# Kernel tuning notes

Measured on AMD Instinct MI355X. Metric: run time of the kernel, lower is better.

The kernel has to match this reference:

```python
import jax, jax.numpy as jnp
import numpy as np

N_NODES = 50000
N_EDGES = 600000
IN_CH = 128
HID_CH = 128
OUT_CH = 64
DEMO = 8
N_GRAPHS = 100


def setup_inputs() -> dict:
    key = jax.random.key(0)
    ks = jax.random.split(key, 16)
    s = 0.02
    inp = {
        "x": jax.random.normal(ks[0], (N_NODES, IN_CH), jnp.float32),
        "edge_index": jax.random.randint(ks[1], (2, N_EDGES), 0, N_NODES, jnp.int32),
        "batch": jnp.sort(jax.random.randint(ks[2], (N_NODES,), 0, N_GRAPHS, jnp.int32)),
        "demographic": jax.random.normal(ks[3], (N_GRAPHS, DEMO), jnp.float32),
        "W1": jax.random.normal(ks[4], (IN_CH, HID_CH), jnp.float32) * s,
        "b1": jnp.zeros((HID_CH,), jnp.float32),
        "W2": jax.random.normal(ks[5], (HID_CH, HID_CH), jnp.float32) * s,
        "b2": jnp.zeros((HID_CH,), jnp.float32),
        "W3": jax.random.normal(ks[6], (HID_CH, OUT_CH), jnp.float32) * s,
        "b3": jnp.zeros((OUT_CH,), jnp.float32),
        "Wf1": jax.random.normal(ks[7], (OUT_CH + DEMO, 64), jnp.float32) * s,
        "bf1": jnp.zeros((64,), jnp.float32),
        "Wf2": jax.random.normal(ks[8], (64, 32), jnp.float32) * s,
        "bf2": jnp.zeros((32,), jnp.float32),
        "Wf3": jax.random.normal(ks[9], (32, 2), jnp.float32) * s,
        "bf3": jnp.zeros((2,), jnp.float32),
    }
    return inp


def _gcn_conv(x, W, b, src, dst, norm, n_nodes):
    # PyG GCNConv: out_i = sum_j norm_ij * (x_j @ W) + b  (self-loops included in src/dst)
    h = x @ W
    msg = h[src] * norm[:, None]
    return jax.ops.segment_sum(msg, dst, num_segments=n_nodes) + b


def reference(x, edge_index, batch, demographic, W1, b1, W2, b2, W3, b3, Wf1, bf1, Wf2, bf2, Wf3, bf3):
    n = x.shape[0]
    # add self-loops
    loop = jnp.arange(n, dtype=edge_index.dtype)
    src = jnp.concatenate([edge_index[0], loop])
    dst = jnp.concatenate([edge_index[1], loop])
    # symmetric degree normalization: deg^{-1/2}[src] * deg^{-1/2}[dst]
    deg = jax.ops.segment_sum(jnp.ones_like(src, jnp.float32), dst, num_segments=n)
    dinv = jnp.where(deg > 0, jax.lax.rsqrt(deg), 0.0)
    norm = dinv[src] * dinv[dst]

    h = jax.nn.relu(_gcn_conv(x, W1, b1, src, dst, norm, n))
    h = jax.nn.relu(_gcn_conv(h, W2, b2, src, dst, norm, n))
    h = jax.nn.relu(_gcn_conv(h, W3, b3, src, dst, norm, n))

    # global mean pool over graphs
    g = demographic.shape[0]
    sums = jax.ops.segment_sum(h, batch, num_segments=g)
    cnts = jax.ops.segment_sum(jnp.ones((n,), jnp.float32), batch, num_segments=g)
    pooled = sums / jnp.maximum(cnts, 1.0)[:, None]

    z = jnp.concatenate([pooled, demographic], axis=1)
    z = jax.nn.relu(z @ Wf1 + bf1)
    z = jax.nn.relu(z @ Wf2 + bf2)
    return z @ Wf3 + bf3
```

## Files before the change

### kernel.cpp

```cpp
#include <hip/hip_runtime.h>


typedef __bf16 bf16x8 __attribute__((ext_vector_type(8)));
typedef float f32x4 __attribute__((ext_vector_type(4)));
typedef float f32x2 __attribute__((ext_vector_type(2)));

__device__ __forceinline__ unsigned char f32_to_fp8(float v) {
    return (unsigned char)(__builtin_amdgcn_cvt_pk_fp8_f32(v, 0.f, 0, false) & 0xff);
}
__device__ __forceinline__ void acc8_fp8(float* a, uint2 u) {
    f32x2 v;
    v = __builtin_amdgcn_cvt_pk_f32_fp8(u.x, false); a[0] += v.x; a[1] += v.y;
    v = __builtin_amdgcn_cvt_pk_f32_fp8(u.x, true);  a[2] += v.x; a[3] += v.y;
    v = __builtin_amdgcn_cvt_pk_f32_fp8(u.y, false); a[4] += v.x; a[5] += v.y;
    v = __builtin_amdgcn_cvt_pk_f32_fp8(u.y, true);  a[6] += v.x; a[7] += v.y;
}

union BF2 {
    __bf16 h[2];
    unsigned u;
};

#define PAD(c) (((c) + 15) & ~15)
#define BCAP 64
#define ECHUNK 4096
#define ECAP 4096
#define BUCKCAP 4096

__device__ __forceinline__ void wpack_block(const float* __restrict__ W,
                                            __bf16* __restrict__ hi,
                                            __bf16* __restrict__ lo, int N, int b, int l) {
    int t = b >> 2, c = b & 3;
    int k0 = c * 32 + (l >> 4) * 8;
    int ncol = t * 16 + (l & 15);
    size_t base = ((size_t)b * 64 + l) * 8;
#pragma unroll
    for (int j = 0; j < 8; j++) {
        float v = W[(size_t)(k0 + j) * N + ncol];
        __bf16 h = (__bf16)v;
        hi[base + j] = h;
        lo[base + j] = (__bf16)(v - (float)h);
    }
}

__global__ __launch_bounds__(1024) void k_bin(const int* __restrict__ src,
                                              const int* __restrict__ dst,
                                              int2* __restrict__ binbuf,
                                              int* __restrict__ bcnt,
                                              const int* __restrict__ batch,
                                              int* __restrict__ gstart,
                                              const float* __restrict__ W1,
                                              const float* __restrict__ W2,
                                              const float* __restrict__ W3,
                                              __bf16* __restrict__ Wp1h, __bf16* __restrict__ Wp1l,
                                              __bf16* __restrict__ Wp2h, __bf16* __restrict__ Wp2l,
                                              __bf16* __restrict__ Wp3h, __bf16* __restrict__ Wp3l,
                                              int E, int EC, int nbuck, int n, int G) {
    int b = blockIdx.x;
    int tid = threadIdx.x;
    if (b < EC) {
        __shared__ int lcur[512];
        for (int i = tid; i < nbuck; i += 1024) lcur[i] = 0;
        __syncthreads();
        int e0 = b * ECHUNK;
        int cntE = E - e0;
        if (cntE > ECHUNK) cntE = ECHUNK;
#pragma unroll
        for (int k = 0; k < 4; k++) {
            int idx = tid + k * 1024;
            if (idx < cntE) {
                int s = src[e0 + idx];
                int d = dst[e0 + idx];
                int bk = d >> 7;
                int slot = atomicAdd(&lcur[bk], 1);
                if (slot < BCAP) {
                    int2 sd = {s, d};
                    binbuf[((size_t)b * nbuck + bk) * BCAP + slot] = sd;
                }
            }
        }
        __syncthreads();
        for (int bk = tid; bk < nbuck; bk += 1024) {
            int c = lcur[bk];
            bcnt[b * nbuck + bk] = (c < BCAP) ? c : BCAP;
        }
        return;
    }
    if (b == EC) {
        int g = tid;
        if (g <= G) {
            int lo = 0, hi = n;
            while (lo < hi) {
                int mid = (lo + hi) >> 1;
                if (batch[mid] < g) lo = mid + 1; else hi = mid;
            }
            gstart[g] = lo;
        }
        return;
    }
    int b64 = (b - EC - 1) * 16 + (tid >> 6);
    int l = tid & 63;
    if (b64 < 32) wpack_block(W1, Wp1h, Wp1l, 128, b64, l);
    else if (b64 < 64) wpack_block(W2, Wp2h, Wp2l, 128, b64 - 32, l);
    else if (b64 < 80) wpack_block(W3, Wp3h, Wp3l, 64, b64 - 64, l);
}

__global__ __launch_bounds__(1024) void k_csr(const int2* __restrict__ binbuf,
                                              const int* __restrict__ bcnt,
                                              float* __restrict__ dinv,
                                              int2* __restrict__ rowspan,
                                              int* __restrict__ col,
                                              unsigned int* __restrict__ tz128,
                                              unsigned int* __restrict__ tz64,
                                              int n, int EC, int nbuck) {
    __shared__ int lcnt[160];
    __shared__ int lpre[161];
    __shared__ int deg[128];
    __shared__ int lloc[129];
    __shared__ int lfill[128];
    __shared__ int sedge[ECAP];
    __shared__ unsigned char redge[ECAP];
    __shared__ int cols_s[BUCKCAP];
    int b = blockIdx.x;
    int tid = threadIdx.x;
    int lane = tid & 63;
    int wid = tid >> 6;
    int r0 = b << 7;
    int r1 = r0 + 128;
    if (r1 > n) r1 = n;
    int nrows = r1 - r0;
    if (b == 0) {
        if (tid < 32) tz128[(size_t)n * 32 + tid] = 0u;
        else if (tid < 48) tz64[(size_t)n * 16 + (tid - 32)] = 0u;
    }
    for (int c = tid; c < EC; c += 1024) lcnt[c] = bcnt[c * nbuck + b];
    if (tid < 128) deg[tid] = 0;
    __syncthreads();
    if (wid == 0) {
        int carry = 0;
        for (int bb = 0; bb < EC; bb += 64) {
            int idx = bb + lane;
            int val = (idx < EC) ? lcnt[idx] : 0;
            int sc = val;
#pragma unroll
            for (int d = 1; d < 64; d <<= 1) {
                int o = __shfl_up(sc, d);
                if (lane >= d) sc += o;
            }
            int grp = __shfl(sc, 63);
            if (idx < EC) lpre[idx] = sc - val + carry;
            carry += grp;
        }
        if (lane == 0) lpre[EC] = carry;
    }
    __syncthreads();
    int T = lpre[EC];
    for (int i = tid; i < T; i += 1024) {
        int lo = 0, hi = EC;
        while (lo < hi) {
            int mid = (lo + hi) >> 1;
            if (lpre[mid + 1] <= i) lo = mid + 1; else hi = mid;
        }
        int j = i - lpre[lo];
        int2 sd = binbuf[((size_t)lo * nbuck + b) * BCAP + j];
        unsigned r = (unsigned)(sd.y - r0);
        bool ok = r < (unsigned)nrows;
        if (ok) atomicAdd(&deg[r], 1);
        if (i < ECAP) {
            sedge[i] = sd.x;
            redge[i] = ok ? (unsigned char)r : (unsigned char)255;
        }
    }
    __syncthreads();
    if (wid == 0) {
        int carry = 0;
#pragma unroll
        for (int bb = 0; bb < 128; bb += 64) {
            int idx = bb + lane;
            int val = (idx < nrows) ? PAD(deg[idx]) : 0;
            int sc = val;
#pragma unroll
            for (int d = 1; d < 64; d <<= 1) {
                int o = __shfl_up(sc, d);
                if (lane >= d) sc += o;
            }
            int grp = __shfl(sc, 63);
            lloc[idx] = sc - val + carry;
            carry += grp;
        }
        if (lane == 0) lloc[128] = carry;
    }
    __syncthreads();
    int base = b * BUCKCAP;
    int tot = lloc[128];
    if (tot > BUCKCAP) tot = BUCKCAP;
    if (tid < nrows) {
        int d = deg[tid];
        lfill[tid] = lloc[tid];
        dinv[r0 + tid] = rsqrtf((float)(d + 1));
        int st = base + lloc[tid];
        int2 sp = {st, st + d};
        rowspan[r0 + tid] = sp;
    }
    for (int i = tid; i < tot; i += 1024) cols_s[i] = n;
    __syncthreads();
    int Tc = (T < ECAP) ? T : ECAP;
    for (int i = tid; i < Tc; i += 1024) {
        int r = redge[i];
        if (r != 255) {
            int pos = atomicAdd(&lfill[r], 1);
            if (pos < BUCKCAP) cols_s[pos] = sedge[i];
        }
    }
    for (int i = ECAP + tid; i < T; i += 1024) {
        int lo = 0, hi = EC;
        while (lo < hi) {
            int mid = (lo + hi) >> 1;
            if (lpre[mid + 1] <= i) lo = mid + 1; else hi = mid;
        }
        int j = i - lpre[lo];
        int2 sd = binbuf[((size_t)lo * nbuck + b) * BCAP + j];
        unsigned r = (unsigned)(sd.y - r0);
        if (r < (unsigned)nrows) {
            int pos = atomicAdd(&lfill[r], 1);
            if (pos < BUCKCAP) cols_s[pos] = sd.x;
        }
    }
    __syncthreads();
    for (int i = tid; i < tot; i += 1024) col[base + i] = cols_s[i];
}

__global__ __launch_bounds__(256) void k_gemm1(const float* __restrict__ A,
                                               const __bf16* __restrict__ Wp_hi,
                                               const __bf16* __restrict__ Wp_lo,
                                               const float* __restrict__ dinv,
                                               unsigned char* __restrict__ Cf8, int n) {
    constexpr int NT = 8;
    constexpr int N = NT * 16;
    int wave = (int)((blockIdx.x * 256u + threadIdx.x) >> 6);
    int lane = threadIdx.x & 63;
    int row0 = wave * 16;
    if (row0 >= n) return;
    int m = lane & 15;
    int q = lane >> 4;
    int row = row0 + m;
    if (row >= n) row = n - 1;
    const float* ap = A + (size_t)row * 128 + q * 8;
    bf16x8 ahi[4], alo[4];
#pragma unroll
    for (int c = 0; c < 4; c++) {
        float4 v0 = *(const float4*)(ap + c * 32);
        float4 v1 = *(const float4*)(ap + c * 32 + 4);
        float vv[8] = {v0.x, v0.y, v0.z, v0.w, v1.x, v1.y, v1.z, v1.w};
#pragma unroll
        for (int j = 0; j < 8; j++) {
            __bf16 h = (__bf16)vv[j];
            ahi[c][j] = h;
            alo[c][j] = (__bf16)(vv[j] - (float)h);
        }
    }
    float dscale[4];
#pragma unroll
    for (int r = 0; r < 4; r++) {
        int rr = row0 + q * 4 + r;
        dscale[r] = dinv[rr < n ? rr : (n - 1)];
    }
#pragma unroll
    for (int t = 0; t < NT; t++) {
        f32x4 acc = {0.f, 0.f, 0.f, 0.f};
#pragma unroll
        for (int c = 0; c < 4; c++) {
            size_t off = ((size_t)(t * 4 + c) * 64 + lane) * 8;
            bf16x8 bh = *(const bf16x8*)(Wp_hi + off);
            bf16x8 bl = *(const bf16x8*)(Wp_lo + off);
            acc = __builtin_amdgcn_mfma_f32_16x16x32_bf16(ahi[c], bh, acc, 0, 0, 0);
            acc = __builtin_amdgcn_mfma_f32_16x16x32_bf16(alo[c], bh, acc, 0, 0, 0);
            acc = __builtin_amdgcn_mfma_f32_16x16x32_bf16(ahi[c], bl, acc, 0, 0, 0);
        }
        int colx = t * 16 + m;
#pragma unroll
        for (int r = 0; r < 4; r++) {
            int orow = row0 + q * 4 + r;
            if (orow < n) Cf8[(size_t)orow * N + colx] = f32_to_fp8(acc[r] * dscale[r]);
        }
    }
}

template <int NT>
__global__ __launch_bounds__(256) void k_gemm_bf16(const __bf16* __restrict__ A,
                                                   const __bf16* __restrict__ Wp_hi,
                                                   const __bf16* __restrict__ Wp_lo,
                                                   const float* __restrict__ dinv,
                                                   unsigned char* __restrict__ Cf8, int n) {
    constexpr int N = NT * 16;
    int wave = (int)((blockIdx.x * 256u + threadIdx.x) >> 6);
    int lane = threadIdx.x & 63;
    int row0 = wave * 16;
    if (row0 >= n) return;
    int m = lane & 15;
    int q = lane >> 4;
    int row = row0 + m;
    if (row >= n) row = n - 1;
    const __bf16* ap = A + (size_t)row * 128 + q * 8;
    bf16x8 a[4];
#pragma unroll
    for (int c = 0; c < 4; c++) a[c] = *(const bf16x8*)(ap + c * 32);
    float dscale[4];
#pragma unroll
    for (int r = 0; r < 4; r++) {
        int rr = row0 + q * 4 + r;
        dscale[r] = dinv[rr < n ? rr : (n - 1)];
    }
#pragma unroll
    for (int t = 0; t < NT; t++) {
        f32x4 acc = {0.f, 0.f, 0.f, 0.f};
#pragma unroll
        for (int c = 0; c < 4; c++) {
            size_t off = ((size_t)(t * 4 + c) * 64 + lane) * 8;
            bf16x8 bh = *(const bf16x8*)(Wp_hi + off);
            bf16x8 bl = *(const bf16x8*)(Wp_lo + off);
            acc = __builtin_amdgcn_mfma_f32_16x16x32_bf16(a[c], bh, acc, 0, 0, 0);
            acc = __builtin_amdgcn_mfma_f32_16x16x32_bf16(a[c], bl, acc, 0, 0, 0);
        }
        int colx = t * 16 + m;
#pragma unroll
        for (int r = 0; r < 4; r++) {
            int orow = row0 + q * 4 + r;
            if (orow < n) Cf8[(size_t)orow * N + colx] = f32_to_fp8(acc[r] * dscale[r]);
        }
    }
}

__global__ __launch_bounds__(256) void k_agg128(const unsigned char* __restrict__ t8,
                                                const int2* __restrict__ rowspan,
                                                const int* __restrict__ col,
                                                const float* __restrict__ dinv,
                                                const float* __restrict__ bias,
                                                unsigned int* __restrict__ out, int n) {
    int w = (int)((blockIdx.x * 256u + threadIdx.x) >> 6);
    int lane = threadIdx.x & 63;
    if (w >= n) return;
    const uint2* t8v = (const uint2*)t8;
    int cg = lane & 15;
    int g = lane >> 4;
    float acc[8] = {0.f, 0.f, 0.f, 0.f, 0.f, 0.f, 0.f, 0.f};
    int2 rs = rowspan[w];
    int p = rs.x;
    int pend = p + ((rs.y - rs.x + 15) & ~15);
    for (; p < pend; p += 16) {
        int c0 = col[p + g];
        int c1 = col[p + 4 + g];
        int c2 = col[p + 8 + g];
        int c3 = col[p + 12 + g];
        uint2 u0 = t8v[((size_t)c0 << 4) + cg];
        uint2 u1 = t8v[((size_t)c1 << 4) + cg];
        uint2 u2 = t8v[((size_t)c2 << 4) + cg];
        uint2 u3 = t8v[((size_t)c3 << 4) + cg];
        acc8_fp8(acc, u0);
        acc8_fp8(acc, u1);
        acc8_fp8(acc, u2);
        acc8_fp8(acc, u3);
    }
#pragma unroll
    for (int j = 0; j < 8; j++) {
        acc[j] += __shfl_xor(acc[j], 16);
        acc[j] += __shfl_xor(acc[j], 32);
    }
    {
        uint2 us = t8v[((size_t)w << 4) + cg];
        float s8[8] = {0.f, 0.f, 0.f, 0.f, 0.f, 0.f, 0.f, 0.f};
        acc8_fp8(s8, us);
#pragma unroll
        for (int j = 0; j < 8; j++) acc[j] += s8[j];
    }
    float di = dinv[w];
    float4 bb0 = *(const float4*)(bias + cg * 8);
    float4 bb1 = *(const float4*)(bias + cg * 8 + 4);
    float bv[8] = {bb0.x, bb0.y, bb0.z, bb0.w, bb1.x, bb1.y, bb1.z, bb1.w};
    BF2 o[4];
#pragma unroll
    for (int j = 0; j < 4; j++) {
        o[j].h[0] = (__bf16)fmaxf(di * acc[2 * j] + bv[2 * j], 0.f);
        o[j].h[1] = (__bf16)fmaxf(di * acc[2 * j + 1] + bv[2 * j + 1], 0.f);
    }
    if (lane < 16) {
        uint4 st = {o[0].u, o[1].u, o[2].u, o[3].u};
        *(uint4*)(out + (size_t)w * 64 + cg * 4) = st;
    }
}

__global__ __launch_bounds__(256) void k_agg64(const unsigned char* __restrict__ t8,
                                               const int2* __restrict__ rowspan,
                                               const int* __restrict__ col,
                                               const float* __restrict__ dinv,
                                               const float* __restrict__ bias,
                                               __bf16* __restrict__ out, int n) {
    int w = (int)((blockIdx.x * 256u + threadIdx.x) >> 6);
    int lane = threadIdx.x & 63;
    if (w >= n) return;
    const uint2* t8v = (const uint2*)t8;
    int cg = lane & 7;
    int g = lane >> 3;
    float acc[8] = {0.f, 0.f, 0.f, 0.f, 0.f, 0.f, 0.f, 0.f};
    int2 rs = rowspan[w];
    int p = rs.x;
    int pend = p + ((rs.y - rs.x + 15) & ~15);
    for (; p < pend; p += 16) {
        int c0 = col[p + g];
        int c1 = col[p + 8 + g];
        uint2 u0 = t8v[((size_t)c0 << 3) + cg];
        uint2 u1 = t8v[((size_t)c1 << 3) + cg];
        acc8_fp8(acc, u0);
        acc8_fp8(acc, u1);
    }
#pragma unroll
    for (int j = 0; j < 8; j++) {
        acc[j] += __shfl_xor(acc[j], 8);
        acc[j] += __shfl_xor(acc[j], 16);
        acc[j] += __shfl_xor(acc[j], 32);
    }
    {
        uint2 us = t8v[((size_t)w << 3) + cg];
        float s8[8] = {0.f, 0.f, 0.f, 0.f, 0.f, 0.f, 0.f, 0.f};
        acc8_fp8(s8, us);
#pragma unroll
        for (int j = 0; j < 8; j++) acc[j] += s8[j];
    }
    float di = dinv[w];
    float4 bb0 = *(const float4*)(bias + cg * 8);
    float4 bb1 = *(const float4*)(bias + cg * 8 + 4);
    float bv[8] = {bb0.x, bb0.y, bb0.z, bb0.w, bb1.x, bb1.y, bb1.z, bb1.w};
    BF2 o[4];
#pragma unroll
    for (int j = 0; j < 4; j++) {
        o[j].h[0] = (__bf16)fmaxf(di * acc[2 * j] + bv[2 * j], 0.f);
        o[j].h[1] = (__bf16)fmaxf(di * acc[2 * j + 1] + bv[2 * j + 1], 0.f);
    }
    if (lane < 8) {
        uint4 st = {o[0].u, o[1].u, o[2].u, o[3].u};
        *(uint4*)((unsigned int*)out + (size_t)w * 32 + cg * 4) = st;
    }
}

__global__ __launch_bounds__(256) void k_poolmlp(const unsigned short* __restrict__ h,
                                                 const int* __restrict__ gstart,
                                                 const float* __restrict__ demo,
                                                 const float* __restrict__ Wf1,
                                                 const float* __restrict__ bf1,
                                                 const float* __restrict__ Wf2,
                                                 const float* __restrict__ bf2,
                                                 const float* __restrict__ Wf3,
                                                 const float* __restrict__ bf3,
                                                 float* __restrict__ out, int G) {
    int g = blockIdx.x;
    int tid = threadIdx.x;
    int lane = tid & 63;
    int wv = tid >> 6;
    int s = gstart[g], e = gstart[g + 1];
    const unsigned* hu = (const unsigned*)h;
    int cg = lane & 15;
    int sub = lane >> 4;
    float acc[4] = {0.f, 0.f, 0.f, 0.f};
    for (int i = s + wv * 4 + sub; i < e; i += 16) {
        uint2 v = *(const uint2*)(hu + ((size_t)i << 5) + cg * 2);
        acc[0] += __uint_as_float(v.x << 16);
        acc[1] += __uint_as_float(v.x & 0xffff0000u);
        acc[2] += __uint_as_float(v.y << 16);
        acc[3] += __uint_as_float(v.y & 0xffff0000u);
    }
#pragma unroll
    for (int j = 0; j < 4; j++) {
        acc[j] += __shfl_xor(acc[j], 16);
        acc[j] += __shfl_xor(acc[j], 32);
    }
    __shared__ float red[4][64];
    __shared__ float zin[72];
    __shared__ float z1[64];
    __shared__ float z2[32];
    if (sub == 0) {
#pragma unroll
        for (int j = 0; j < 4; j++) red[wv][cg * 4 + j] = acc[j];
    }
    if (tid >= 64 && tid < 72) zin[tid] = demo[g * 8 + (tid - 64)];
    __syncthreads();
    if (tid < 64) {
        float v = red[0][tid] + red[1][tid] + red[2][tid] + red[3][tid];
        zin[tid] = v / fmaxf((float)(e - s), 1.0f);
    }
    __syncthreads();
    if (tid < 64) {
        float a = bf1[tid];
        for (int k = 0; k < 72; k++) a += zin[k] * Wf1[k * 64 + tid];
        z1[tid] = fmaxf(a, 0.f);
    }
    __syncthreads();
    if (tid < 32) {
        float a2 = bf2[tid];
        for (int k = 0; k < 64; k++) a2 += z1[k] * Wf2[k * 32 + tid];
        z2[tid] = fmaxf(a2, 0.f);
    }
    __syncthreads();
    if (tid < 2) {
        float a3 = bf3[tid];
        for (int k = 0; k < 32; k++) a3 += z2[k] * Wf3[k * 2 + tid];
        out[g * 2 + tid] = a3;
    }
}

extern "C" void kernel_launch(void* const* d_in, const int* in_sizes, int n_in,
                              void* d_out, int out_size, void* d_ws, size_t ws_size,
                              hipStream_t stream) {
    const float* x    = (const float*)d_in[0];
    const int*   ei   = (const int*)d_in[1];
    const int*   batch= (const int*)d_in[2];
    const float* demo = (const float*)d_in[3];
    const float* W1   = (const float*)d_in[4];
    const float* b1   = (const float*)d_in[5];
    const float* W2   = (const float*)d_in[6];
    const float* b2   = (const float*)d_in[7];
    const float* W3   = (const float*)d_in[8];
    const float* b3   = (const float*)d_in[9];
    const float* Wf1  = (const float*)d_in[10];
    const float* bf1  = (const float*)d_in[11];
    const float* Wf2  = (const float*)d_in[12];
    const float* bf2  = (const float*)d_in[13];
    const float* Wf3  = (const float*)d_in[14];
    const float* bf3  = (const float*)d_in[15];
    float* out = (float*)d_out;

    const int n = in_sizes[0] / 128;
    const int E = in_sizes[1] / 2;
    const int G = in_sizes[3] / 8;
    const int EC = (E + ECHUNK - 1) / ECHUNK;
    const int nbuck = (n + 127) / 128;

    char* ws = (char*)d_ws;
    auto alloc = [&](size_t bytes) {
        char* p = ws;
        ws += (bytes + 255) & ~(size_t)255;
        return p;
    };
    float*  dinv    = (float*)alloc((size_t)n * 4);
    int2*   rowspan = (int2*)alloc((size_t)n * 8);
    int*    col     = (int*)alloc((size_t)nbuck * BUCKCAP * 4 + 256);
    int2*   binbuf  = (int2*)alloc((size_t)EC * nbuck * BCAP * 8);
    int*    bcnt    = (int*)alloc((size_t)EC * nbuck * 4);
    unsigned char* tbf  = (unsigned char*)alloc((size_t)(n + 1) * 128);
    __bf16* hbuf    = (__bf16*)alloc((size_t)n * 128 * 2);
    unsigned char* t3bf = (unsigned char*)alloc((size_t)(n + 1) * 64);
    __bf16* h3      = (__bf16*)alloc((size_t)n * 64 * 2);
    __bf16* Wp1h    = (__bf16*)alloc(128 * 128 * 2);
    __bf16* Wp1l    = (__bf16*)alloc(128 * 128 * 2);
    __bf16* Wp2h    = (__bf16*)alloc(128 * 128 * 2);
    __bf16* Wp2l    = (__bf16*)alloc(128 * 128 * 2);
    __bf16* Wp3h    = (__bf16*)alloc(128 * 64 * 2);
    __bf16* Wp3l    = (__bf16*)alloc(128 * 64 * 2);
    int*    gstart  = (int*)alloc((size_t)(G + 1) * 4);

    const int* srcv = ei;
    const int* dstv = ei + E;

    int waves = (n + 15) / 16;
    int gemm_blocks = (waves + 3) / 4;
    int agg_blocks = (int)(((size_t)n * 64 + 255) / 256);

    k_bin<<<EC + 1 + 5, 1024, 0, stream>>>(srcv, dstv, binbuf, bcnt, batch, gstart,
                                           W1, W2, W3, Wp1h, Wp1l, Wp2h, Wp2l,
                                           Wp3h, Wp3l, E, EC, nbuck, n, G);
    k_csr<<<nbuck, 1024, 0, stream>>>(binbuf, bcnt, dinv, rowspan, col,
                                      (unsigned int*)tbf, (unsigned int*)t3bf,
                                      n, EC, nbuck);
    k_gemm1<<<gemm_blocks, 256, 0, stream>>>(x, Wp1h, Wp1l, dinv, tbf, n);
    k_agg128<<<agg_blocks, 256, 0, stream>>>(tbf, rowspan, col,
                                             dinv, b1, (unsigned int*)hbuf, n);
    k_gemm_bf16<8><<<gemm_blocks, 256, 0, stream>>>(hbuf, Wp2h, Wp2l, dinv, tbf, n);
    k_agg128<<<agg_blocks, 256, 0, stream>>>(tbf, rowspan, col,
                                             dinv, b2, (unsigned int*)hbuf, n);
    k_gemm_bf16<4><<<gemm_blocks, 256, 0, stream>>>(hbuf, Wp3h, Wp3l, dinv, t3bf, n);
    k_agg64<<<agg_blocks, 256, 0, stream>>>(t3bf, rowspan, col,
                                            dinv, b3, h3, n);

    k_poolmlp<<<G, 256, 0, stream>>>((const unsigned short*)h3, gstart, demo,
                                     Wf1, bf1, Wf2, bf2, Wf3, bf3, out, G);
}
```

Measured before the change: 222.7 us.

## Fuse GCN aggregation with next-layer GEMM and fold mean pooling into last aggregation

Each aggregation now runs inside a 16-row block that stages the bf16 relu outputs in shared memory and immediately multiplies them by the next layer's weights, so the intermediate hbuf never goes to global memory. A second fp8 ping-pong buffer is added because the fused kernel reads from one buffer and writes the next. The final 64-wide aggregation accumulates relu outputs directly into per-graph pooled sums with float atomics, and the pool kernel is reduced to an MLP. The cost is fewer waves per block for the gather, one block per 16 rows, and heavy atomic contention on only 100 graph rows.

```diff
diff --git a/kernel.cpp b/kernel.cpp
--- a/kernel.cpp
+++ b/kernel.cpp
@@ -110,9 +110,11 @@
                                               float* __restrict__ dinv,
                                               int2* __restrict__ rowspan,
                                               int* __restrict__ col,
-                                              unsigned int* __restrict__ tz128,
+                                              unsigned int* __restrict__ tzA,
+                                              unsigned int* __restrict__ tzB,
                                               unsigned int* __restrict__ tz64,
-                                              int n, int EC, int nbuck) {
+                                              float* __restrict__ pooled,
+                                              int n, int EC, int nbuck, int G) {
     __shared__ int lcnt[160];
     __shared__ int lpre[161];
     __shared__ int deg[128];
@@ -130,8 +132,10 @@
     if (r1 > n) r1 = n;
     int nrows = r1 - r0;
     if (b == 0) {
-        if (tid < 32) tz128[(size_t)n * 32 + tid] = 0u;
-        else if (tid < 48) tz64[(size_t)n * 16 + (tid - 32)] = 0u;
+        if (tid < 32) tzA[(size_t)n * 32 + tid] = 0u;
+        else if (tid < 64) tzB[(size_t)n * 32 + (tid - 32)] = 0u;
+        else if (tid < 80) tz64[(size_t)n * 16 + (tid - 64)] = 0u;
+        for (int i = tid; i < G * 64; i += 1024) pooled[i] = 0.f;
     }
     for (int c = tid; c < EC; c += 1024) lcnt[c] = bcnt[c * nbuck + b];
     if (tid < 128) deg[tid] = 0;
@@ -287,32 +291,93 @@
 }
 
 template <int NT>
-__global__ __launch_bounds__(256) void k_gemm_bf16(const __bf16* __restrict__ A,
-                                                   const __bf16* __restrict__ Wp_hi,
-                                                   const __bf16* __restrict__ Wp_lo,
-                                                   const float* __restrict__ dinv,
-                                                   unsigned char* __restrict__ Cf8, int n) {
+__global__ __launch_bounds__(256) void k_aggemm(const unsigned char* __restrict__ t8,
+                                                const int2* __restrict__ rowspan,
+                                                const int* __restrict__ col,
+                                                const float* __restrict__ dinv,
+                                                const float* __restrict__ bias,
+                                                const __bf16* __restrict__ Wp_hi,
+                                                const __bf16* __restrict__ Wp_lo,
+                                                unsigned char* __restrict__ Cf8, int n) {
     constexpr int N = NT * 16;
-    int wave = (int)((blockIdx.x * 256u + threadIdx.x) >> 6);
-    int lane = threadIdx.x & 63;
-    int row0 = wave * 16;
-    if (row0 >= n) return;
+    __shared__ __bf16 As[16][136];
+    int row0 = blockIdx.x * 16;
+    int tid = threadIdx.x;
+    int lane = tid & 63;
+    int v = tid >> 6;
+    const uint2* t8v = (const uint2*)t8;
+    int cg = lane & 15;
+    int g = lane >> 4;
+    float4 bb0 = *(const float4*)(bias + cg * 8);
+    float4 bb1 = *(const float4*)(bias + cg * 8 + 4);
+    float bv[8] = {bb0.x, bb0.y, bb0.z, bb0.w, bb1.x, bb1.y, bb1.z, bb1.w};
+#pragma unroll 1
+    for (int r = 0; r < 4; r++) {
+        int lr = v * 4 + r;
+        int w = row0 + lr;
+        if (w < n) {
+            float acc[8] = {0.f, 0.f, 0.f, 0.f, 0.f, 0.f, 0.f, 0.f};
+            int2 rs = rowspan[w];
+            int p = rs.x;
+            int pend = p + ((rs.y - rs.x + 15) & ~15);
+            for (; p < pend; p += 16) {
+                int c0 = col[p + g];
+                int c1 = col[p + 4 + g];
+                int c2 = col[p + 8 + g];
+                int c3 = col[p + 12 + g];
+                uint2 u0 = t8v[((size_t)c0 << 4) + cg];
+                uint2 u1 = t8v[((size_t)c1 << 4) + cg];
+                uint2 u2 = t8v[((size_t)c2 << 4) + cg];
+                uint2 u3 = t8v[((size_t)c3 << 4) + cg];
+                acc8_fp8(acc, u0);
+                acc8_fp8(acc, u1);
+                acc8_fp8(acc, u2);
+                acc8_fp8(acc, u3);
+            }
+#pragma unroll
+            for (int j = 0; j < 8; j++) {
+                acc[j] += __shfl_xor(acc[j], 16);
+                acc[j] += __shfl_xor(acc[j], 32);
+            }
+            {
+                uint2 us = t8v[((size_t)w << 4) + cg];
+                float s8[8] = {0.f, 0.f, 0.f, 0.f, 0.f, 0.f, 0.f, 0.f};
+                acc8_fp8(s8, us);
+#pragma unroll
+                for (int j = 0; j < 8; j++) acc[j] += s8[j];
+            }
+            float di = dinv[w];
+            BF2 o[4];
+#pragma unroll
+            for (int j = 0; j < 4; j++) {
+                o[j].h[0] = (__bf16)fmaxf(di * acc[2 * j] + bv[2 * j], 0.f);
+                o[j].h[1] = (__bf16)fmaxf(di * acc[2 * j + 1] + bv[2 * j + 1], 0.f);
+            }
+            if (lane < 16) {
+                uint4 st = {o[0].u, o[1].u, o[2].u, o[3].u};
+                *(uint4*)&As[lr][cg * 8] = st;
+            }
+        } else if (lane < 16) {
+            uint4 z = {0u, 0u, 0u, 0u};
+            *(uint4*)&As[lr][cg * 8] = z;
+        }
+    }
+    __syncthreads();
     int m = lane & 15;
     int q = lane >> 4;
-    int row = row0 + m;
-    if (row >= n) row = n - 1;
-    const __bf16* ap = A + (size_t)row * 128 + q * 8;
     bf16x8 a[4];
 #pragma unroll
-    for (int c = 0; c < 4; c++) a[c] = *(const bf16x8*)(ap + c * 32);
+    for (int c = 0; c < 4; c++) a[c] = *(const bf16x8*)&As[m][q * 8 + c * 32];
     float dscale[4];
 #pragma unroll
     for (int r = 0; r < 4; r++) {
         int rr = row0 + q * 4 + r;
         dscale[r] = dinv[rr < n ? rr : (n - 1)];
     }
-#pragma unroll
-    for (int t = 0; t < NT; t++) {
+    constexpr int TPW = NT / 4;
+#pragma unroll
+    for (int tt = 0; tt < TPW; tt++) {
+        int t = v * TPW + tt;
         f32x4 acc = {0.f, 0.f, 0.f, 0.f};
 #pragma unroll
         for (int c = 0; c < 4; c++) {
@@ -331,70 +396,13 @@
     }
 }
 
-__global__ __launch_bounds__(256) void k_agg128(const unsigned char* __restrict__ t8,
-                                                const int2* __restrict__ rowspan,
-                                                const int* __restrict__ col,
-                                                const float* __restrict__ dinv,
-                                                const float* __restrict__ bias,
-                                                unsigned int* __restrict__ out, int n) {
-    int w = (int)((blockIdx.x * 256u + threadIdx.x) >> 6);
-    int lane = threadIdx.x & 63;
-    if (w >= n) return;
-    const uint2* t8v = (const uint2*)t8;
-    int cg = lane & 15;
-    int g = lane >> 4;
-    float acc[8] = {0.f, 0.f, 0.f, 0.f, 0.f, 0.f, 0.f, 0.f};
-    int2 rs = rowspan[w];
-    int p = rs.x;
-    int pend = p + ((rs.y - rs.x + 15) & ~15);
-    for (; p < pend; p += 16) {
-        int c0 = col[p + g];
-        int c1 = col[p + 4 + g];
-        int c2 = col[p + 8 + g];
-        int c3 = col[p + 12 + g];
-        uint2 u0 = t8v[((size_t)c0 << 4) + cg];
-        uint2 u1 = t8v[((size_t)c1 << 4) + cg];
-        uint2 u2 = t8v[((size_t)c2 << 4) + cg];
-        uint2 u3 = t8v[((size_t)c3 << 4) + cg];
-        acc8_fp8(acc, u0);
-        acc8_fp8(acc, u1);
-        acc8_fp8(acc, u2);
-        acc8_fp8(acc, u3);
-    }
-#pragma unroll
-    for (int j = 0; j < 8; j++) {
-        acc[j] += __shfl_xor(acc[j], 16);
-        acc[j] += __shfl_xor(acc[j], 32);
-    }
-    {
-        uint2 us = t8v[((size_t)w << 4) + cg];
-        float s8[8] = {0.f, 0.f, 0.f, 0.f, 0.f, 0.f, 0.f, 0.f};
-        acc8_fp8(s8, us);
-#pragma unroll
-        for (int j = 0; j < 8; j++) acc[j] += s8[j];
-    }
-    float di = dinv[w];
-    float4 bb0 = *(const float4*)(bias + cg * 8);
-    float4 bb1 = *(const float4*)(bias + cg * 8 + 4);
-    float bv[8] = {bb0.x, bb0.y, bb0.z, bb0.w, bb1.x, bb1.y, bb1.z, bb1.w};
-    BF2 o[4];
-#pragma unroll
-    for (int j = 0; j < 4; j++) {
-        o[j].h[0] = (__bf16)fmaxf(di * acc[2 * j] + bv[2 * j], 0.f);
-        o[j].h[1] = (__bf16)fmaxf(di * acc[2 * j + 1] + bv[2 * j + 1], 0.f);
-    }
-    if (lane < 16) {
-        uint4 st = {o[0].u, o[1].u, o[2].u, o[3].u};
-        *(uint4*)(out + (size_t)w * 64 + cg * 4) = st;
-    }
-}
-
-__global__ __launch_bounds__(256) void k_agg64(const unsigned char* __restrict__ t8,
-                                               const int2* __restrict__ rowspan,
-                                               const int* __restrict__ col,
-                                               const float* __restrict__ dinv,
-                                               const float* __restrict__ bias,
-                                               __bf16* __restrict__ out, int n) {
+__global__ __launch_bounds__(256) void k_agg3pool(const unsigned char* __restrict__ t8,
+                                                  const int2* __restrict__ rowspan,
+                                                  const int* __restrict__ col,
+                                                  const float* __restrict__ dinv,
+                                                  const float* __restrict__ bias,
+                                                  const int* __restrict__ batch,
+                                                  float* __restrict__ pooled, int n) {
     int w = (int)((blockIdx.x * 256u + threadIdx.x) >> 6);
     int lane = threadIdx.x & 63;
     if (w >= n) return;
@@ -426,67 +434,37 @@
 #pragma unroll
         for (int j = 0; j < 8; j++) acc[j] += s8[j];
     }
-    float di = dinv[w];
-    float4 bb0 = *(const float4*)(bias + cg * 8);
-    float4 bb1 = *(const float4*)(bias + cg * 8 + 4);
-    float bv[8] = {bb0.x, bb0.y, bb0.z, bb0.w, bb1.x, bb1.y, bb1.z, bb1.w};
-    BF2 o[4];
-#pragma unroll
-    for (int j = 0; j < 4; j++) {
-        o[j].h[0] = (__bf16)fmaxf(di * acc[2 * j] + bv[2 * j], 0.f);
-        o[j].h[1] = (__bf16)fmaxf(di * acc[2 * j + 1] + bv[2 * j + 1], 0.f);
-    }
     if (lane < 8) {
-        uint4 st = {o[0].u, o[1].u, o[2].u, o[3].u};
-        *(uint4*)((unsigned int*)out + (size_t)w * 32 + cg * 4) = st;
-    }
-}
-
-__global__ __launch_bounds__(256) void k_poolmlp(const unsigned short* __restrict__ h,
-                                                 const int* __restrict__ gstart,
-                                                 const float* __restrict__ demo,
-                                                 const float* __restrict__ Wf1,
-                                                 const float* __restrict__ bf1,
-                                                 const float* __restrict__ Wf2,
-                                                 const float* __restrict__ bf2,
-                                                 const float* __restrict__ Wf3,
-                                                 const float* __restrict__ bf3,
-                                                 float* __restrict__ out, int G) {
+        float di = dinv[w];
+        int gId = batch[w];
+        float4 bb0 = *(const float4*)(bias + cg * 8);
+        float4 bb1 = *(const float4*)(bias + cg * 8 + 4);
+        float bv[8] = {bb0.x, bb0.y, bb0.z, bb0.w, bb1.x, bb1.y, bb1.z, bb1.w};
+        float* pp = pooled + (size_t)gId * 64 + cg * 8;
+#pragma unroll
+        for (int j = 0; j < 8; j++)
+            atomicAdd(&pp[j], fmaxf(di * acc[j] + bv[j], 0.f));
+    }
+}
+
+__global__ __launch_bounds__(256) void k_mlp(const float* __restrict__ pooled,
+                                             const int* __restrict__ gstart,
+                                             const float* __restrict__ demo,
+                                             const float* __restrict__ Wf1,
+                                             const float* __restrict__ bf1,
+                                             const float* __restrict__ Wf2,
+                                             const float* __restrict__ bf2,
+                                             const float* __restrict__ Wf3,
+                                             const float* __restrict__ bf3,
+                                             float* __restrict__ out, int G) {
     int g = blockIdx.x;
     int tid = threadIdx.x;
-    int lane = tid & 63;
-    int wv = tid >> 6;
     int s = gstart[g], e = gstart[g + 1];
-    const unsigned* hu = (const unsigned*)h;
-    int cg = lane & 15;
-    int sub = lane >> 4;
-    float acc[4] = {0.f, 0.f, 0.f, 0.f};
-    for (int i = s + wv * 4 + sub; i < e; i += 16) {
-        uint2 v = *(const uint2*)(hu + ((size_t)i << 5) + cg * 2);
-        acc[0] += __uint_as_float(v.x << 16);
-        acc[1] += __uint_as_float(v.x & 0xffff0000u);
-        acc[2] += __uint_as_float(v.y << 16);
-        acc[3] += __uint_as_float(v.y & 0xffff0000u);
-    }
-#pragma unroll
-    for (int j = 0; j < 4; j++) {
-        acc[j] += __shfl_xor(acc[j], 16);
-        acc[j] += __shfl_xor(acc[j], 32);
-    }
-    __shared__ float red[4][64];
     __shared__ float zin[72];
     __shared__ float z1[64];
     __shared__ float z2[32];
-    if (sub == 0) {
-#pragma unroll
-        for (int j = 0; j < 4; j++) red[wv][cg * 4 + j] = acc[j];
-    }
-    if (tid >= 64 && tid < 72) zin[tid] = demo[g * 8 + (tid - 64)];
-    __syncthreads();
-    if (tid < 64) {
-        float v = red[0][tid] + red[1][tid] + red[2][tid] + red[3][tid];
-        zin[tid] = v / fmaxf((float)(e - s), 1.0f);
-    }
+    if (tid < 64) zin[tid] = pooled[g * 64 + tid] / fmaxf((float)(e - s), 1.0f);
+    else if (tid < 72) zin[tid] = demo[g * 8 + (tid - 64)];
     __syncthreads();
     if (tid < 64) {
         float a = bf1[tid];
@@ -546,9 +524,9 @@
     int2*   binbuf  = (int2*)alloc((size_t)EC * nbuck * BCAP * 8);
     int*    bcnt    = (int*)alloc((size_t)EC * nbuck * 4);
     unsigned char* tbf  = (unsigned char*)alloc((size_t)(n + 1) * 128);
-    __bf16* hbuf    = (__bf16*)alloc((size_t)n * 128 * 2);
+    unsigned char* tbf2 = (unsigned char*)alloc((size_t)(n + 1) * 128);
     unsigned char* t3bf = (unsigned char*)alloc((size_t)(n + 1) * 64);
-    __bf16* h3      = (__bf16*)alloc((size_t)n * 64 * 2);
+    float*  pooled  = (float*)alloc((size_t)G * 64 * 4);
     __bf16* Wp1h    = (__bf16*)alloc(128 * 128 * 2);
     __bf16* Wp1l    = (__bf16*)alloc(128 * 128 * 2);
     __bf16* Wp2h    = (__bf16*)alloc(128 * 128 * 2);
@@ -562,24 +540,22 @@
 
     int waves = (n + 15) / 16;
     int gemm_blocks = (waves + 3) / 4;
+    int fuse_blocks = waves;
     int agg_blocks = (int)(((size_t)n * 64 + 255) / 256);
 
     k_bin<<<EC + 1 + 5, 1024, 0, stream>>>(srcv, dstv, binbuf, bcnt, batch, gstart,
                                            W1, W2, W3, Wp1h, Wp1l, Wp2h, Wp2l,
                                            Wp3h, Wp3l, E, EC, nbuck, n, G);
     k_csr<<<nbuck, 1024, 0, stream>>>(binbuf, bcnt, dinv, rowspan, col,
-                                      (unsigned int*)tbf, (unsigned int*)t3bf,
-                                      n, EC, nbuck);
+                                      (unsigned int*)tbf, (unsigned int*)tbf2,
+                                      (unsigned int*)t3bf, pooled, n, EC, nbuck, G);
     k_gemm1<<<gemm_blocks, 256, 0, stream>>>(x, Wp1h, Wp1l, dinv, tbf, n);
-    k_agg128<<<agg_blocks, 256, 0, stream>>>(tbf, rowspan, col,
-                                             dinv, b1, (unsigned int*)hbuf, n);
-    k_gemm_bf16<8><<<gemm_blocks, 256, 0, stream>>>(hbuf, Wp2h, Wp2l, dinv, tbf, n);
-    k_agg128<<<agg_blocks, 256, 0, stream>>>(tbf, rowspan, col,
-                                             dinv, b2, (unsigned int*)hbuf, n);
-    k_gemm_bf16<4><<<gemm_blocks, 256, 0, stream>>>(hbuf, Wp3h, Wp3l, dinv, t3bf, n);
-    k_agg64<<<agg_blocks, 256, 0, stream>>>(t3bf, rowspan, col,
-                                            dinv, b3, h3, n);
-
-    k_poolmlp<<<G, 256, 0, stream>>>((const unsigned short*)h3, gstart, demo,
-                                     Wf1, bf1, Wf2, bf2, Wf3, bf3, out, G);
-}
+    k_aggemm<8><<<fuse_blocks, 256, 0, stream>>>(tbf, rowspan, col, dinv, b1,
+                                                 Wp2h, Wp2l, tbf2, n);
+    k_aggemm<4><<<fuse_blocks, 256, 0, stream>>>(tbf2, rowspan, col, dinv, b2,
+                                                 Wp3h, Wp3l, t3bf, n);
+    k_agg3pool<<<agg_blocks, 256, 0, stream>>>(t3bf, rowspan, col, dinv, b3,
+                                               batch, pooled, n);
+    k_mlp<<<G, 256, 0, stream>>>(pooled, gstart, demo,
+                                 Wf1, bf1, Wf2, bf2, Wf3, bf3, out, G);
+}
```

After: 498.1 us. +123.7%, slower.
